# Optimization experiments

Measured on AMD Instinct MI355X. Metric: run time of the kernel, lower is better.

The kernel has to match this reference:

```python
import jax, jax.numpy as jnp
import numpy as np
import math

HEADS = 8
DIM_HEAD = 64

def setup_inputs() -> dict:
    key = jax.random.key(0)
    ks = jax.random.split(key, 6)
    B, L, D = 2, 2048, 512
    Ls = 1936
    inner = HEADS * DIM_HEAD  # 512
    x = jax.random.normal(ks[0], (B, L, D), dtype=jnp.float32)
    positions = jax.random.normal(ks[1], (B, Ls, 2), dtype=jnp.float32) * 10.0
    w_qkv = jax.random.normal(ks[2], (3 * inner, D), dtype=jnp.float32) * (1.0 / math.sqrt(D))
    w_out = jax.random.normal(ks[3], (D, inner), dtype=jnp.float32) * (1.0 / math.sqrt(inner))
    b_out = jnp.zeros((D,), dtype=jnp.float32)
    log_sigma = jnp.full((HEADS,), math.log(3.0), dtype=jnp.float32)
    global_bias = jnp.float32(0.0)
    return {"x": x, "positions": positions, "w_qkv": w_qkv, "w_out": w_out,
            "b_out": b_out, "log_sigma": log_sigma, "global_bias": global_bias,
            "num_spatial": Ls}

def reference(x, positions, w_qkv, w_out, b_out, log_sigma, global_bias, num_spatial):
    B, L, D = x.shape
    H, Dh = HEADS, DIM_HEAD
    scale = Dh ** (-0.5)
    # qkv projection: [B,L,3*H*Dh] -> q,k,v each [B,H,L,Dh]
    qkv = jnp.einsum('bld,ed->ble', x, w_qkv)
    q, k, v = jnp.split(qkv, 3, axis=-1)
    def heads(t):
        return t.reshape(B, L, H, Dh).transpose(0, 2, 1, 3)
    q, k, v = heads(q), heads(k), heads(v)
    attn = jnp.einsum('bhid,bhjd->bhij', q, k) * scale  # [B,H,L,L]
    # Gaussian distance bias on the spatial block, global_bias elsewhere
    Ls = num_spatial
    diff = positions[:, :, None, :] - positions[:, None, :, :]  # [B,Ls,Ls,2]
    dist_sq = jnp.sum(diff * diff, axis=-1)                     # [B,Ls,Ls]
    sigma_sq = jnp.exp(log_sigma) ** 2                          # [H]
    spatial_bias = -dist_sq[:, None] / (2.0 * sigma_sq[None, :, None, None])  # [B,H,Ls,Ls]
    full_bias = jnp.full((B, H, L, L), global_bias, dtype=x.dtype)
    full_bias = full_bias.at[:, :, :Ls, :Ls].set(spatial_bias)
    attn = jax.nn.softmax(attn + full_bias, axis=-1)
    out = jnp.einsum('bhij,bhjd->bhid', attn, v)  # [B,H,L,Dh]
    out = out.transpose(0, 2, 1, 3).reshape(B, L, H * Dh)
    return jnp.einsum('ble,de->bld', out, w_out) + b_out
```

## Files before the change

### kernel.cpp

```cpp
#include <hip/hip_runtime.h>
#include <stdint.h>
#include <stddef.h>

#define NB   2
#define NL   2048
#define ND   512
#define NH   8
#define DH   64
#define LOG2E 1.44269504f
#define NIT  16
#define RG_TOT 32768

typedef __attribute__((ext_vector_type(8))) short bf16x8;
typedef __attribute__((ext_vector_type(4))) float f32x4;

__device__ __forceinline__ unsigned short f2bf(float f) {
  union { float f; unsigned int u; } c; c.f = f;
  unsigned int u = c.u;
  unsigned int r = u + 0x7fffu + ((u >> 16) & 1u);
  return (unsigned short)(r >> 16);
}

__device__ __forceinline__ float fexp2(float x) {
#if __has_builtin(__builtin_amdgcn_exp2f)
  return __builtin_amdgcn_exp2f(x);
#else
  return exp2f(x);
#endif
}

__device__ __forceinline__ void gl_lds16(const unsigned short* g, unsigned short* l) {
#if __has_builtin(__builtin_amdgcn_global_load_lds)
  __builtin_amdgcn_global_load_lds(
      (const __attribute__((address_space(1))) unsigned int*)g,
      (__attribute__((address_space(3))) unsigned int*)l, 16, 0, 0);
#else
  *(uint4*)l = *(const uint4*)g;
#endif
}

#define XC  524288
#define WQC 196608
#define WOC 65536
__global__ void cvt_f32_bf16(const float* __restrict__ x, const float* __restrict__ wq,
                             const float* __restrict__ wo, unsigned short* __restrict__ xb,
                             unsigned short* __restrict__ wqb, unsigned short* __restrict__ wob) {
  int idx = blockIdx.x * 256 + threadIdx.x;
  const float* src; unsigned short* dst; int off;
  if (idx < XC)            { src = x;  dst = xb;  off = idx; }
  else if (idx < XC + WQC) { src = wq; dst = wqb; off = idx - XC; }
  else                     { src = wo; dst = wob; off = idx - XC - WQC; }
  float4 f = ((const float4*)src)[off];
  ushort4 o;
  o.x = f2bf(f.x); o.y = f2bf(f.y); o.z = f2bf(f.z); o.w = f2bf(f.w);
  ((ushort4*)dst)[off] = o;
}

template<int MODE>
__global__ __launch_bounds__(256, 2) void gemm_bf16(
    const unsigned short* __restrict__ A, const unsigned short* __restrict__ Bm,
    const float* __restrict__ bias,
    unsigned short* __restrict__ qo, unsigned short* __restrict__ ko,
    unsigned short* __restrict__ vo, float* __restrict__ out, int K)
{
  __shared__ __align__(16) unsigned short As[128 * 32];
  __shared__ __align__(16) unsigned short Bs[128 * 32];
  const int tid = threadIdx.x, wid = tid >> 6, lane = tid & 63;
  const int quad = lane >> 4, l15 = lane & 15;
  const int m0 = blockIdx.x * 128, n0 = blockIdx.y * 128;
  const int wm = (wid >> 1) * 64, wn = (wid & 1) * 64;

  f32x4 acc[4][4];
#pragma unroll
  for (int a = 0; a < 4; ++a)
#pragma unroll
    for (int b = 0; b < 4; ++b)
#pragma unroll
      for (int z = 0; z < 4; ++z) acc[a][b][z] = 0.f;

  for (int k0 = 0; k0 < K; k0 += 32) {
#pragma unroll
    for (int p = 0; p < 2; ++p) {
      int c = p * 256 + wid * 64 + lane;
      int row = c >> 2, off = c & 3;
      gl_lds16(A  + (size_t)(m0 + row) * K + k0 + off * 8, &As[c * 8]);
      gl_lds16(Bm + (size_t)(n0 + row) * K + k0 + off * 8, &Bs[c * 8]);
    }
    __syncthreads();
    bf16x8 af[4], bfr[4];
#pragma unroll
    for (int mb = 0; mb < 4; ++mb)
      af[mb] = *(const bf16x8*)&As[(wm + mb * 16 + l15) * 32 + quad * 8];
#pragma unroll
    for (int nb = 0; nb < 4; ++nb)
      bfr[nb] = *(const bf16x8*)&Bs[(wn + nb * 16 + l15) * 32 + quad * 8];
#pragma unroll
    for (int mb = 0; mb < 4; ++mb)
#pragma unroll
      for (int nb = 0; nb < 4; ++nb)
        acc[mb][nb] = __builtin_amdgcn_mfma_f32_16x16x32_bf16(af[mb], bfr[nb], acc[mb][nb], 0, 0, 0);
    __syncthreads();
  }

  const float QSCALE = 0.125f * LOG2E;
#pragma unroll
  for (int mb = 0; mb < 4; ++mb) {
#pragma unroll
    for (int r = 0; r < 4; ++r) {
      int m  = m0 + wm + mb * 16 + quad * 4 + r;
      int bb = m >> 11;
      int ll = m & 2047;
#pragma unroll
      for (int nb = 0; nb < 4; ++nb) {
        int n = n0 + wn + nb * 16 + l15;
        float v = acc[mb][nb][r];
        if (MODE == 0) {
          int s  = n >> 9;
          int hh = (n >> 6) & 7;
          int dh = n & 63;
          size_t base = (((size_t)bb * NH + hh) * NL + ll) * DH + dh;
          if (s == 0)      qo[base] = f2bf(v * QSCALE);
          else if (s == 1) ko[base] = f2bf(v);
          else             vo[base] = f2bf(v);
        } else {
          out[(size_t)m * ND + n] = v + bias[n];
        }
      }
    }
  }
}

__global__ __launch_bounds__(256) void transpose_v(const unsigned short* __restrict__ v,
                                                   unsigned short* __restrict__ vT) {
  __shared__ unsigned short T[64][74];
  const int l0 = blockIdx.x * 64;
  const int bh = blockIdx.y;
  const unsigned short* src = v + ((size_t)bh * NL + l0) * DH;
  unsigned short* dst = vT + (size_t)bh * DH * NL;
#pragma unroll
  for (int p = 0; p < 2; ++p) {
    int c = p * 256 + threadIdx.x;
    int row = c >> 3, seg = c & 7;
    *(uint4*)&T[row][seg * 8] = *(const uint4*)(src + row * DH + seg * 8);
  }
  __syncthreads();
#pragma unroll
  for (int p = 0; p < 2; ++p) {
    int c = p * 256 + threadIdx.x;
    int drow = c >> 3, lseg = c & 7;
    unsigned short u[8];
#pragma unroll
    for (int z = 0; z < 8; ++z) u[z] = T[lseg * 8 + z][drow];
    *(uint4*)(dst + (size_t)drow * NL + l0 + lseg * 8) = *(uint4*)u;
  }
}

__global__ __launch_bounds__(256, 2) void flash_kernel(
    const unsigned short* __restrict__ qb, const unsigned short* __restrict__ kb,
    const unsigned short* __restrict__ vTb, const float* __restrict__ positions,
    const float* __restrict__ log_sigma, const float* __restrict__ gbias_p,
    const int* __restrict__ ns_p, float* __restrict__ Pbuf, float* __restrict__ rsbuf)
{
  const int it = blockIdx.x >> 1;
  const int js = blockIdx.x & 1;
  const int h  = blockIdx.y;
  const int b  = blockIdx.z;
  const int i0 = it * 128;
  const int jbase = js * (NL / 2);
  const int Ls = ns_p[0];
  const float gb = gbias_p[0];
  const float sig = __expf(log_sigma[h]);
  const float inv2s2 = 0.5f / (sig * sig);
  const float CI = LOG2E * inv2s2;
  const float A2 = 2.0f * CI;
  const float CG = LOG2E * gb * 0.5f;
  const float C8N = -8.0f * LOG2E;

  const int tid  = threadIdx.x;
  const int wid  = tid >> 6;
  const int lane = tid & 63;
  const int quad = lane >> 4;
  const int l15  = lane & 15;

  __shared__ __align__(16) unsigned short Ks[64][72];
  __shared__ __align__(16) unsigned short Vt[64][72];
  __shared__ __align__(16) unsigned short Ps[128][72];
  __shared__ __align__(16) float4 pjc[64];

  const size_t bh = (size_t)b * NH + h;
  const unsigned short* qbase  = qb  + (bh * NL + i0) * DH;
  const unsigned short* kbase  = kb  + bh * NL * DH;
  const unsigned short* vtbase = vTb + bh * DH * NL;

  bf16x8 af[2][2];
#pragma unroll
  for (int mb = 0; mb < 2; ++mb)
#pragma unroll
    for (int kc = 0; kc < 2; ++kc)
      af[mb][kc] = *(const bf16x8*)(qbase + (size_t)(wid * 32 + mb * 16 + l15) * DH + kc * 32 + quad * 8);

  float pix_[2][4], piy_[2][4], riCm[2][4], ispf[2][4];
#pragma unroll
  for (int mb = 0; mb < 2; ++mb)
#pragma unroll
    for (int r = 0; r < 4; ++r) {
      int ig = i0 + wid * 32 + mb * 16 + quad * 4 + r;
      float px = 0.f, py = 0.f, sf = 0.f, rc = 0.f;
      if (ig < Ls) {
        float2 p2 = *(const float2*)(positions + ((size_t)b * Ls + ig) * 2);
        px = p2.x; py = p2.y; sf = 1.f;
        rc = -(CI * (px * px + py * py)) - CG;
      }
      pix_[mb][r] = px; piy_[mb][r] = py; ispf[mb][r] = sf; riCm[mb][r] = rc;
    }

  f32x4 accO[2][4];
  float rsum[2][4];
#pragma unroll
  for (int mb = 0; mb < 2; ++mb) {
#pragma unroll
    for (int nb = 0; nb < 4; ++nb)
#pragma unroll
      for (int z = 0; z < 4; ++z) accO[mb][nb][z] = 0.f;
#pragma unroll
    for (int r = 0; r < 4; ++r) rsum[mb][r] = 0.f;
  }

  uint4 kr[2], vr[2];
  float2 pr = make_float2(0.f, 0.f);
  {
#pragma unroll
    for (int p = 0; p < 2; ++p) {
      int c = p * 256 + tid;
      int row = c >> 3, off = c & 7;
      kr[p] = *(const uint4*)(kbase  + (size_t)(jbase + row) * DH + off * 8);
      vr[p] = *(const uint4*)(vtbase + (size_t)row * NL + jbase + off * 8);
    }
    if (tid < 64 && (jbase + tid) < Ls)
      pr = *(const float2*)(positions + ((size_t)b * Ls + jbase + tid) * 2);
  }

  for (int jt = 0; jt < 16; ++jt) {
    const int j0 = jbase + jt * 64;
    __syncthreads();

#pragma unroll
    for (int p = 0; p < 2; ++p) {
      int c = p * 256 + tid;
      int row = c >> 3, off = c & 7;
      *(uint4*)&Ks[row][off * 8] = kr[p];
      *(uint4*)&Vt[row][off * 8] = vr[p];
    }
    if (tid < 64) {
      bool jsp = (j0 + tid) < Ls;
      float px = jsp ? pr.x : 0.f, py = jsp ? pr.y : 0.f;
      float rc = jsp ? (-(CI * (px * px + py * py)) - CG) : 0.f;
      pjc[tid] = make_float4(A2 * px, A2 * py, rc, 0.f);
    }
    __syncthreads();

    if (jt + 1 < 16) {
      const int jn = jbase + (jt + 1) * 64;
#pragma unroll
      for (int p = 0; p < 2; ++p) {
        int c = p * 256 + tid;
        int row = c >> 3, off = c & 7;
        kr[p] = *(const uint4*)(kbase  + (size_t)(jn + row) * DH + off * 8);
        vr[p] = *(const uint4*)(vtbase + (size_t)row * NL + jn + off * 8);
      }
      if (tid < 64 && (jn + tid) < Ls)
        pr = *(const float2*)(positions + ((size_t)b * Ls + jn + tid) * 2);
    }

    f32x4 accS[2][4];
#pragma unroll
    for (int mb = 0; mb < 2; ++mb)
#pragma unroll
      for (int nb = 0; nb < 4; ++nb)
#pragma unroll
        for (int z = 0; z < 4; ++z) accS[mb][nb][z] = 0.f;
#pragma unroll
    for (int nb = 0; nb < 4; ++nb) {
      bf16x8 b0 = *(const bf16x8*)&Ks[nb * 16 + l15][quad * 8];
      bf16x8 b1 = *(const bf16x8*)&Ks[nb * 16 + l15][32 + quad * 8];
#pragma unroll
      for (int mb = 0; mb < 2; ++mb) {
        accS[mb][nb] = __builtin_amdgcn_mfma_f32_16x16x32_bf16(af[mb][0], b0, accS[mb][nb], 0, 0, 0);
        accS[mb][nb] = __builtin_amdgcn_mfma_f32_16x16x32_bf16(af[mb][1], b1, accS[mb][nb], 0, 0, 0);
      }
    }

    float4 pc[4]; float jspf_[4];
#pragma unroll
    for (int nb = 0; nb < 4; ++nb) {
      pc[nb] = pjc[nb * 16 + l15];
      jspf_[nb] = ((j0 + nb * 16 + l15) < Ls) ? 1.f : 0.f;
    }
#pragma unroll
    for (int mb = 0; mb < 2; ++mb)
#pragma unroll
      for (int nb = 0; nb < 4; ++nb)
#pragma unroll
        for (int r = 0; r < 4; ++r) {
          float t = accS[mb][nb][r] + C8N;
          t = __builtin_fmaf(ispf[mb][r], pc[nb].z, t);
          t = __builtin_fmaf(jspf_[nb], riCm[mb][r], t);
          t = __builtin_fmaf(piy_[mb][r], pc[nb].y, t);
          t = __builtin_fmaf(pix_[mb][r], pc[nb].x, t);
          float p = fexp2(t);
          rsum[mb][r] += p;
          Ps[wid * 32 + mb * 16 + quad * 4 + r][nb * 16 + l15] = f2bf(p);
        }

    bf16x8 pf[2][2];
#pragma unroll
    for (int mb = 0; mb < 2; ++mb) {
      pf[mb][0] = *(const bf16x8*)&Ps[wid * 32 + mb * 16 + l15][quad * 8];
      pf[mb][1] = *(const bf16x8*)&Ps[wid * 32 + mb * 16 + l15][32 + quad * 8];
    }
#pragma unroll
    for (int nb = 0; nb < 4; ++nb) {
      bf16x8 v0 = *(const bf16x8*)&Vt[nb * 16 + l15][quad * 8];
      bf16x8 v1 = *(const bf16x8*)&Vt[nb * 16 + l15][32 + quad * 8];
#pragma unroll
      for (int mb = 0; mb < 2; ++mb) {
        accO[mb][nb] = __builtin_amdgcn_mfma_f32_16x16x32_bf16(pf[mb][0], v0, accO[mb][nb], 0, 0, 0);
        accO[mb][nb] = __builtin_amdgcn_mfma_f32_16x16x32_bf16(pf[mb][1], v1, accO[mb][nb], 0, 0, 0);
      }
    }
  }

#pragma unroll
  for (int mb = 0; mb < 2; ++mb)
#pragma unroll
    for (int r = 0; r < 4; ++r) {
      float v = rsum[mb][r];
      v += __shfl_xor(v, 1);
      v += __shfl_xor(v, 2);
      v += __shfl_xor(v, 4);
      v += __shfl_xor(v, 8);
      rsum[mb][r] = v;
    }
  const size_t rgbase = (bh * NIT + it) * 128;
  const size_t poff = (size_t)js * RG_TOT * DH;
#pragma unroll
  for (int mb = 0; mb < 2; ++mb)
#pragma unroll
    for (int r = 0; r < 4; ++r) {
      int row = wid * 32 + mb * 16 + quad * 4 + r;
#pragma unroll
      for (int nb = 0; nb < 4; ++nb)
        Pbuf[poff + (rgbase + row) * DH + nb * 16 + l15] = accO[mb][nb][r];
      if (l15 == 0)
        rsbuf[(size_t)js * RG_TOT + rgbase + row] = rsum[mb][r];
    }
}

__global__ __launch_bounds__(256) void combine_kernel(const float* __restrict__ Pbuf,
                                                      const float* __restrict__ rsbuf,
                                                      unsigned short* __restrict__ attnb) {
  int idx = blockIdx.x * 256 + threadIdx.x;
  int rg = idx >> 4, c4 = idx & 15;
  const float4* p4 = (const float4*)Pbuf;
  float4 p0 = p4[(size_t)rg * 16 + c4];
  float4 p1 = p4[(size_t)RG_TOT * 16 + (size_t)rg * 16 + c4];
  float rs = 1.0f / (rsbuf[rg] + rsbuf[RG_TOT + rg]);
  int bhm = rg >> 11;
  int l   = rg & 2047;
  int bb  = bhm >> 3, hh = bhm & 7;
  ushort4 o;
  o.x = f2bf((p0.x + p1.x) * rs);
  o.y = f2bf((p0.y + p1.y) * rs);
  o.z = f2bf((p0.z + p1.z) * rs);
  o.w = f2bf((p0.w + p1.w) * rs);
  *(ushort4*)&attnb[(((size_t)bb * NL + l) * ND) + hh * DH + c4 * 4] = o;
}

extern "C" void kernel_launch(void* const* d_in, const int* in_sizes, int n_in,
                              void* d_out, int out_size, void* d_ws, size_t ws_size,
                              hipStream_t stream) {
  const float* x         = (const float*)d_in[0];
  const float* positions = (const float*)d_in[1];
  const float* w_qkv     = (const float*)d_in[2];
  const float* w_out     = (const float*)d_in[3];
  const float* b_out     = (const float*)d_in[4];
  const float* log_sigma = (const float*)d_in[5];
  const float* gbias     = (const float*)d_in[6];
  const int*   ns        = (const int*)d_in[7];

  unsigned short* ws = (unsigned short*)d_ws;
  unsigned short* xb  = ws;
  unsigned short* wqb = xb  + 2097152;
  unsigned short* wob = wqb + 786432;
  unsigned short* qbf = wob + 262144;
  unsigned short* kbf = qbf + 2097152;
  unsigned short* vbf = kbf + 2097152;
  unsigned short* vTf = vbf + 2097152;
  float* Pbuf  = (float*)(vTf + 2097152);
  float* rsbuf = Pbuf + (size_t)2 * RG_TOT * DH;

  cvt_f32_bf16<<<(XC + WQC + WOC) / 256, 256, 0, stream>>>(x, w_qkv, w_out, xb, wqb, wob);

  dim3 g1(NB * NL / 128, (3 * NH * DH) / 128);
  gemm_bf16<0><<<g1, 256, 0, stream>>>(xb, wqb, nullptr, qbf, kbf, vbf, nullptr, ND);

  dim3 gt(NL / 64, NB * NH);
  transpose_v<<<gt, 256, 0, stream>>>(vbf, vTf);

  dim3 g2(NIT * 2, NH, NB);
  flash_kernel<<<g2, 256, 0, stream>>>(qbf, kbf, vTf, positions, log_sigma, gbias, ns,
                                       Pbuf, rsbuf);

  combine_kernel<<<RG_TOT * 16 / 256, 256, 0, stream>>>(Pbuf, rsbuf, xb);

  dim3 g3(NB * NL / 128, ND / 128);
  gemm_bf16<1><<<g3, 256, 0, stream>>>(xb, wob, b_out, nullptr, nullptr, nullptr,
                                       (float*)d_out, NH * DH);
}
```

Baseline: 167.1 us.

## Transpose flash tiles, drop shared K/V staging, pad positions, vectorize GEMM epilogues

The flash kernel now computes S^T (keys as the MFMA A operand, queries as B) so each lane owns one query row. K and V^T fragments are read straight from global memory instead of being staged through shared memory, which removes both block-wide barriers per tile. Only a small per-wave P buffer stays in LDS. The Gaussian bias is computed directly from a zero-padded positions array that the conversion kernel now builds. Both GEMMs swap operand order so the epilogue writes ushort4/float4 vectors instead of scalars; the trade-off is that global K/V reloads now depend on L2 and lose the register prefetch double-buffering.

```diff
diff --git a/kernel.cpp b/kernel.cpp
--- a/kernel.cpp
+++ b/kernel.cpp
@@ -8,7 +8,6 @@
 #define NH   8
 #define DH   64
 #define LOG2E 1.44269504f
-#define NIT  16
 #define RG_TOT 32768
 
 typedef __attribute__((ext_vector_type(8))) short bf16x8;
@@ -42,18 +41,36 @@
 #define XC  524288
 #define WQC 196608
 #define WOC 65536
+#define TOTC (XC + WQC + WOC)
 __global__ void cvt_f32_bf16(const float* __restrict__ x, const float* __restrict__ wq,
-                             const float* __restrict__ wo, unsigned short* __restrict__ xb,
-                             unsigned short* __restrict__ wqb, unsigned short* __restrict__ wob) {
+                             const float* __restrict__ wo, const float* __restrict__ positions,
+                             const int* __restrict__ ns_p,
+                             unsigned short* __restrict__ xb, unsigned short* __restrict__ wqb,
+                             unsigned short* __restrict__ wob, float* __restrict__ pospad) {
   int idx = blockIdx.x * 256 + threadIdx.x;
-  const float* src; unsigned short* dst; int off;
-  if (idx < XC)            { src = x;  dst = xb;  off = idx; }
-  else if (idx < XC + WQC) { src = wq; dst = wqb; off = idx - XC; }
-  else                     { src = wo; dst = wob; off = idx - XC - WQC; }
-  float4 f = ((const float4*)src)[off];
-  ushort4 o;
-  o.x = f2bf(f.x); o.y = f2bf(f.y); o.z = f2bf(f.z); o.w = f2bf(f.w);
-  ((ushort4*)dst)[off] = o;
+  if (idx < TOTC) {
+    const float* src; unsigned short* dst; int off;
+    if (idx < XC)            { src = x;  dst = xb;  off = idx; }
+    else if (idx < XC + WQC) { src = wq; dst = wqb; off = idx - XC; }
+    else                     { src = wo; dst = wob; off = idx - XC - WQC; }
+    float4 f = ((const float4*)src)[off];
+    ushort4 o;
+    o.x = f2bf(f.x); o.y = f2bf(f.y); o.z = f2bf(f.z); o.w = f2bf(f.w);
+    ((ushort4*)dst)[off] = o;
+  } else {
+    int i2 = idx - TOTC;
+    if (i2 < NB * 1024) {
+      int b = i2 >> 10;
+      int jj = (i2 & 1023) * 2;
+      int Ls = ns_p[0];
+      float4 o = make_float4(0.f, 0.f, 0.f, 0.f);
+      if (jj < Ls) { o.x = positions[((size_t)b * Ls + jj) * 2];
+                     o.y = positions[((size_t)b * Ls + jj) * 2 + 1]; }
+      if (jj + 1 < Ls) { o.z = positions[((size_t)b * Ls + jj + 1) * 2];
+                         o.w = positions[((size_t)b * Ls + jj + 1) * 2 + 1]; }
+      *(float4*)&pospad[((size_t)b * NL + jj) * 2] = o;
+    }
+  }
 }
 
 template<int MODE>
@@ -105,26 +122,35 @@
   const float QSCALE = 0.125f * LOG2E;
 #pragma unroll
   for (int mb = 0; mb < 4; ++mb) {
-#pragma unroll
-    for (int r = 0; r < 4; ++r) {
-      int m  = m0 + wm + mb * 16 + quad * 4 + r;
-      int bb = m >> 11;
-      int ll = m & 2047;
+    int e0 = m0 + wm + mb * 16 + quad * 4;
+    if (MODE == 0) {
+      int s   = e0 >> 9;
+      int hh  = (e0 >> 6) & 7;
+      int dh0 = e0 & 63;
+      unsigned short* dst = (s == 0) ? qo : ((s == 1) ? ko : vo);
+      float sc = (s == 0) ? QSCALE : 1.0f;
 #pragma unroll
       for (int nb = 0; nb < 4; ++nb) {
-        int n = n0 + wn + nb * 16 + l15;
-        float v = acc[mb][nb][r];
-        if (MODE == 0) {
-          int s  = n >> 9;
-          int hh = (n >> 6) & 7;
-          int dh = n & 63;
-          size_t base = (((size_t)bb * NH + hh) * NL + ll) * DH + dh;
-          if (s == 0)      qo[base] = f2bf(v * QSCALE);
-          else if (s == 1) ko[base] = f2bf(v);
-          else             vo[base] = f2bf(v);
-        } else {
-          out[(size_t)m * ND + n] = v + bias[n];
-        }
+        int token = n0 + wn + nb * 16 + l15;
+        int bb = token >> 11, ll = token & 2047;
+        ushort4 o;
+        o.x = f2bf(acc[mb][nb][0] * sc);
+        o.y = f2bf(acc[mb][nb][1] * sc);
+        o.z = f2bf(acc[mb][nb][2] * sc);
+        o.w = f2bf(acc[mb][nb][3] * sc);
+        *(ushort4*)&dst[(((size_t)bb * NH + hh) * NL + ll) * DH + dh0] = o;
+      }
+    } else {
+      float4 bv = *(const float4*)&bias[e0];
+#pragma unroll
+      for (int nb = 0; nb < 4; ++nb) {
+        int token = n0 + wn + nb * 16 + l15;
+        float4 o;
+        o.x = acc[mb][nb][0] + bv.x;
+        o.y = acc[mb][nb][1] + bv.y;
+        o.z = acc[mb][nb][2] + bv.z;
+        o.w = acc[mb][nb][3] + bv.w;
+        *(float4*)&out[(size_t)token * ND + e0] = o;
       }
     }
   }
@@ -157,7 +183,7 @@
 
 __global__ __launch_bounds__(256, 2) void flash_kernel(
     const unsigned short* __restrict__ qb, const unsigned short* __restrict__ kb,
-    const unsigned short* __restrict__ vTb, const float* __restrict__ positions,
+    const unsigned short* __restrict__ vTb, const float* __restrict__ pospad,
     const float* __restrict__ log_sigma, const float* __restrict__ gbias_p,
     const int* __restrict__ ns_p, float* __restrict__ Pbuf, float* __restrict__ rsbuf)
 {
@@ -168,12 +194,10 @@
   const int i0 = it * 128;
   const int jbase = js * (NL / 2);
   const int Ls = ns_p[0];
-  const float gb = gbias_p[0];
+  const float gb  = gbias_p[0];
   const float sig = __expf(log_sigma[h]);
-  const float inv2s2 = 0.5f / (sig * sig);
-  const float CI = LOG2E * inv2s2;
-  const float A2 = 2.0f * CI;
-  const float CG = LOG2E * gb * 0.5f;
+  const float CI  = LOG2E * 0.5f / (sig * sig);
+  const float LGB = LOG2E * gb;
   const float C8N = -8.0f * LOG2E;
 
   const int tid  = threadIdx.x;
@@ -182,178 +206,122 @@
   const int quad = lane >> 4;
   const int l15  = lane & 15;
 
-  __shared__ __align__(16) unsigned short Ks[64][72];
-  __shared__ __align__(16) unsigned short Vt[64][72];
-  __shared__ __align__(16) unsigned short Ps[128][72];
-  __shared__ __align__(16) float4 pjc[64];
+  __shared__ __align__(16) unsigned short Pls[4][2][16][72];
 
   const size_t bh = (size_t)b * NH + h;
-  const unsigned short* qbase  = qb  + (bh * NL + i0) * DH;
+  const unsigned short* qbase  = qb  + (bh * NL + i0 + wid * 32) * DH;
   const unsigned short* kbase  = kb  + bh * NL * DH;
   const unsigned short* vtbase = vTb + bh * DH * NL;
-
-  bf16x8 af[2][2];
-#pragma unroll
-  for (int mb = 0; mb < 2; ++mb)
+  const float* posb = pospad + (size_t)b * NL * 2;
+
+  bf16x8 qf[2][2];
+  float pix[2], piy[2], ispf[2];
+#pragma unroll
+  for (int ib = 0; ib < 2; ++ib) {
 #pragma unroll
     for (int kc = 0; kc < 2; ++kc)
-      af[mb][kc] = *(const bf16x8*)(qbase + (size_t)(wid * 32 + mb * 16 + l15) * DH + kc * 32 + quad * 8);
-
-  float pix_[2][4], piy_[2][4], riCm[2][4], ispf[2][4];
-#pragma unroll
-  for (int mb = 0; mb < 2; ++mb)
-#pragma unroll
-    for (int r = 0; r < 4; ++r) {
-      int ig = i0 + wid * 32 + mb * 16 + quad * 4 + r;
-      float px = 0.f, py = 0.f, sf = 0.f, rc = 0.f;
-      if (ig < Ls) {
-        float2 p2 = *(const float2*)(positions + ((size_t)b * Ls + ig) * 2);
-        px = p2.x; py = p2.y; sf = 1.f;
-        rc = -(CI * (px * px + py * py)) - CG;
-      }
-      pix_[mb][r] = px; piy_[mb][r] = py; ispf[mb][r] = sf; riCm[mb][r] = rc;
-    }
-
-  f32x4 accO[2][4];
-  float rsum[2][4];
-#pragma unroll
-  for (int mb = 0; mb < 2; ++mb) {
-#pragma unroll
-    for (int nb = 0; nb < 4; ++nb)
-#pragma unroll
-      for (int z = 0; z < 4; ++z) accO[mb][nb][z] = 0.f;
-#pragma unroll
-    for (int r = 0; r < 4; ++r) rsum[mb][r] = 0.f;
-  }
-
-  uint4 kr[2], vr[2];
-  float2 pr = make_float2(0.f, 0.f);
-  {
-#pragma unroll
-    for (int p = 0; p < 2; ++p) {
-      int c = p * 256 + tid;
-      int row = c >> 3, off = c & 7;
-      kr[p] = *(const uint4*)(kbase  + (size_t)(jbase + row) * DH + off * 8);
-      vr[p] = *(const uint4*)(vtbase + (size_t)row * NL + jbase + off * 8);
-    }
-    if (tid < 64 && (jbase + tid) < Ls)
-      pr = *(const float2*)(positions + ((size_t)b * Ls + jbase + tid) * 2);
-  }
+      qf[ib][kc] = *(const bf16x8*)(qbase + (size_t)(ib * 16 + l15) * DH + kc * 32 + quad * 8);
+    int ig = i0 + wid * 32 + ib * 16 + l15;
+    float2 p2 = *(const float2*)(posb + (size_t)ig * 2);
+    pix[ib] = p2.x; piy[ib] = p2.y;
+    ispf[ib] = (ig < Ls) ? 1.f : 0.f;
+  }
+
+  f32x4 accO[4][2];
+  float rsum[2];
+#pragma unroll
+  for (int d = 0; d < 4; ++d)
+#pragma unroll
+    for (int ib = 0; ib < 2; ++ib)
+#pragma unroll
+      for (int z = 0; z < 4; ++z) accO[d][ib][z] = 0.f;
+  rsum[0] = 0.f; rsum[1] = 0.f;
 
   for (int jt = 0; jt < 16; ++jt) {
     const int j0 = jbase + jt * 64;
-    __syncthreads();
-
-#pragma unroll
-    for (int p = 0; p < 2; ++p) {
-      int c = p * 256 + tid;
-      int row = c >> 3, off = c & 7;
-      *(uint4*)&Ks[row][off * 8] = kr[p];
-      *(uint4*)&Vt[row][off * 8] = vr[p];
-    }
-    if (tid < 64) {
-      bool jsp = (j0 + tid) < Ls;
-      float px = jsp ? pr.x : 0.f, py = jsp ? pr.y : 0.f;
-      float rc = jsp ? (-(CI * (px * px + py * py)) - CG) : 0.f;
-      pjc[tid] = make_float4(A2 * px, A2 * py, rc, 0.f);
-    }
-    __syncthreads();
-
-    if (jt + 1 < 16) {
-      const int jn = jbase + (jt + 1) * 64;
-#pragma unroll
-      for (int p = 0; p < 2; ++p) {
-        int c = p * 256 + tid;
-        int row = c >> 3, off = c & 7;
-        kr[p] = *(const uint4*)(kbase  + (size_t)(jn + row) * DH + off * 8);
-        vr[p] = *(const uint4*)(vtbase + (size_t)row * NL + jn + off * 8);
-      }
-      if (tid < 64 && (jn + tid) < Ls)
-        pr = *(const float2*)(positions + ((size_t)b * Ls + jn + tid) * 2);
-    }
-
-    f32x4 accS[2][4];
-#pragma unroll
-    for (int mb = 0; mb < 2; ++mb)
-#pragma unroll
-      for (int nb = 0; nb < 4; ++nb)
-#pragma unroll
-        for (int z = 0; z < 4; ++z) accS[mb][nb][z] = 0.f;
-#pragma unroll
-    for (int nb = 0; nb < 4; ++nb) {
-      bf16x8 b0 = *(const bf16x8*)&Ks[nb * 16 + l15][quad * 8];
-      bf16x8 b1 = *(const bf16x8*)&Ks[nb * 16 + l15][32 + quad * 8];
-#pragma unroll
-      for (int mb = 0; mb < 2; ++mb) {
-        accS[mb][nb] = __builtin_amdgcn_mfma_f32_16x16x32_bf16(af[mb][0], b0, accS[mb][nb], 0, 0, 0);
-        accS[mb][nb] = __builtin_amdgcn_mfma_f32_16x16x32_bf16(af[mb][1], b1, accS[mb][nb], 0, 0, 0);
-      }
-    }
-
-    float4 pc[4]; float jspf_[4];
-#pragma unroll
-    for (int nb = 0; nb < 4; ++nb) {
-      pc[nb] = pjc[nb * 16 + l15];
-      jspf_[nb] = ((j0 + nb * 16 + l15) < Ls) ? 1.f : 0.f;
-    }
-#pragma unroll
-    for (int mb = 0; mb < 2; ++mb)
-#pragma unroll
-      for (int nb = 0; nb < 4; ++nb)
+
+    bf16x8 kf[4][2];
+#pragma unroll
+    for (int jb = 0; jb < 4; ++jb)
+#pragma unroll
+      for (int kc = 0; kc < 2; ++kc)
+        kf[jb][kc] = *(const bf16x8*)(kbase + (size_t)(j0 + jb * 16 + l15) * DH + kc * 32 + quad * 8);
+
+    f32x4 accS[4][2];
+#pragma unroll
+    for (int jb = 0; jb < 4; ++jb)
+#pragma unroll
+      for (int ib = 0; ib < 2; ++ib) {
+#pragma unroll
+        for (int z = 0; z < 4; ++z) accS[jb][ib][z] = 0.f;
+        accS[jb][ib] = __builtin_amdgcn_mfma_f32_16x16x32_bf16(kf[jb][0], qf[ib][0], accS[jb][ib], 0, 0, 0);
+        accS[jb][ib] = __builtin_amdgcn_mfma_f32_16x16x32_bf16(kf[jb][1], qf[ib][1], accS[jb][ib], 0, 0, 0);
+      }
+
+#pragma unroll
+    for (int jb = 0; jb < 4; ++jb) {
+      int jrow = j0 + jb * 16 + quad * 4;
+      float4 pA = *(const float4*)(posb + (size_t)jrow * 2);
+      float4 pB = *(const float4*)(posb + (size_t)jrow * 2 + 4);
+      float px[4] = {pA.x, pA.z, pB.x, pB.z};
+      float py[4] = {pA.y, pA.w, pB.y, pB.w};
+      float jok[4];
+#pragma unroll
+      for (int r = 0; r < 4; ++r) jok[r] = (jrow + r < Ls) ? 1.f : 0.f;
+#pragma unroll
+      for (int ib = 0; ib < 2; ++ib) {
+        float p[4];
 #pragma unroll
         for (int r = 0; r < 4; ++r) {
-          float t = accS[mb][nb][r] + C8N;
-          t = __builtin_fmaf(ispf[mb][r], pc[nb].z, t);
-          t = __builtin_fmaf(jspf_[nb], riCm[mb][r], t);
-          t = __builtin_fmaf(piy_[mb][r], pc[nb].y, t);
-          t = __builtin_fmaf(pix_[mb][r], pc[nb].x, t);
-          float p = fexp2(t);
-          rsum[mb][r] += p;
-          Ps[wid * 32 + mb * 16 + quad * 4 + r][nb * 16 + l15] = f2bf(p);
+          float dx = pix[ib] - px[r];
+          float dy = piy[ib] - py[r];
+          float d2 = __builtin_fmaf(dx, dx, dy * dy);
+          float u  = __builtin_fmaf(CI, d2, LGB);
+          float m  = jok[r] * ispf[ib];
+          float t  = __builtin_fmaf(-m, u, accS[jb][ib][r] + C8N);
+          p[r] = fexp2(t);
         }
-
-    bf16x8 pf[2][2];
-#pragma unroll
-    for (int mb = 0; mb < 2; ++mb) {
-      pf[mb][0] = *(const bf16x8*)&Ps[wid * 32 + mb * 16 + l15][quad * 8];
-      pf[mb][1] = *(const bf16x8*)&Ps[wid * 32 + mb * 16 + l15][32 + quad * 8];
-    }
-#pragma unroll
-    for (int nb = 0; nb < 4; ++nb) {
-      bf16x8 v0 = *(const bf16x8*)&Vt[nb * 16 + l15][quad * 8];
-      bf16x8 v1 = *(const bf16x8*)&Vt[nb * 16 + l15][32 + quad * 8];
-#pragma unroll
-      for (int mb = 0; mb < 2; ++mb) {
-        accO[mb][nb] = __builtin_amdgcn_mfma_f32_16x16x32_bf16(pf[mb][0], v0, accO[mb][nb], 0, 0, 0);
-        accO[mb][nb] = __builtin_amdgcn_mfma_f32_16x16x32_bf16(pf[mb][1], v1, accO[mb][nb], 0, 0, 0);
-      }
-    }
-  }
-
-#pragma unroll
-  for (int mb = 0; mb < 2; ++mb)
-#pragma unroll
-    for (int r = 0; r < 4; ++r) {
-      float v = rsum[mb][r];
-      v += __shfl_xor(v, 1);
-      v += __shfl_xor(v, 2);
-      v += __shfl_xor(v, 4);
-      v += __shfl_xor(v, 8);
-      rsum[mb][r] = v;
-    }
-  const size_t rgbase = (bh * NIT + it) * 128;
-  const size_t poff = (size_t)js * RG_TOT * DH;
-#pragma unroll
-  for (int mb = 0; mb < 2; ++mb)
-#pragma unroll
-    for (int r = 0; r < 4; ++r) {
-      int row = wid * 32 + mb * 16 + quad * 4 + r;
-#pragma unroll
-      for (int nb = 0; nb < 4; ++nb)
-        Pbuf[poff + (rgbase + row) * DH + nb * 16 + l15] = accO[mb][nb][r];
-      if (l15 == 0)
-        rsbuf[(size_t)js * RG_TOT + rgbase + row] = rsum[mb][r];
-    }
+        rsum[ib] += (p[0] + p[1]) + (p[2] + p[3]);
+        uint2 w;
+        w.x = (uint32_t)f2bf(p[0]) | ((uint32_t)f2bf(p[1]) << 16);
+        w.y = (uint32_t)f2bf(p[2]) | ((uint32_t)f2bf(p[3]) << 16);
+        *(uint2*)&Pls[wid][ib][l15][jb * 16 + quad * 4] = w;
+      }
+    }
+
+    bf16x8 pbf[2][2];
+#pragma unroll
+    for (int ib = 0; ib < 2; ++ib)
+#pragma unroll
+      for (int pp = 0; pp < 2; ++pp)
+        pbf[ib][pp] = *(const bf16x8*)&Pls[wid][ib][l15][pp * 32 + quad * 8];
+#pragma unroll
+    for (int dhb = 0; dhb < 4; ++dhb)
+#pragma unroll
+      for (int pp = 0; pp < 2; ++pp) {
+        bf16x8 vf = *(const bf16x8*)(vtbase + (size_t)(dhb * 16 + l15) * NL + j0 + pp * 32 + quad * 8);
+#pragma unroll
+        for (int ib = 0; ib < 2; ++ib)
+          accO[dhb][ib] = __builtin_amdgcn_mfma_f32_16x16x32_bf16(vf, pbf[ib][pp], accO[dhb][ib], 0, 0, 0);
+      }
+  }
+
+#pragma unroll
+  for (int ib = 0; ib < 2; ++ib) {
+    float v = rsum[ib];
+    v += __shfl_xor(v, 16);
+    v += __shfl_xor(v, 32);
+    int ig = i0 + wid * 32 + ib * 16 + l15;
+    if (quad == 0)
+      rsbuf[(size_t)js * RG_TOT + bh * NL + ig] = v;
+#pragma unroll
+    for (int dhb = 0; dhb < 4; ++dhb) {
+      float4 o;
+      o.x = accO[dhb][ib][0]; o.y = accO[dhb][ib][1];
+      o.z = accO[dhb][ib][2]; o.w = accO[dhb][ib][3];
+      *(float4*)&Pbuf[((size_t)js * RG_TOT + bh * NL + ig) * DH + dhb * 16 + quad * 4] = o;
+    }
+  }
 }
 
 __global__ __launch_bounds__(256) void combine_kernel(const float* __restrict__ Pbuf,
@@ -396,24 +364,26 @@
   unsigned short* kbf = qbf + 2097152;
   unsigned short* vbf = kbf + 2097152;
   unsigned short* vTf = vbf + 2097152;
-  float* Pbuf  = (float*)(vTf + 2097152);
-  float* rsbuf = Pbuf + (size_t)2 * RG_TOT * DH;
-
-  cvt_f32_bf16<<<(XC + WQC + WOC) / 256, 256, 0, stream>>>(x, w_qkv, w_out, xb, wqb, wob);
-
-  dim3 g1(NB * NL / 128, (3 * NH * DH) / 128);
-  gemm_bf16<0><<<g1, 256, 0, stream>>>(xb, wqb, nullptr, qbf, kbf, vbf, nullptr, ND);
+  float* Pbuf   = (float*)(vTf + 2097152);
+  float* rsbuf  = Pbuf + (size_t)2 * RG_TOT * DH;
+  float* pospad = rsbuf + 2 * RG_TOT;
+
+  cvt_f32_bf16<<<(TOTC + NB * 1024 + 255) / 256, 256, 0, stream>>>(
+      x, w_qkv, w_out, positions, ns, xb, wqb, wob, pospad);
+
+  dim3 g1((3 * NH * DH) / 128, NB * NL / 128);
+  gemm_bf16<0><<<g1, 256, 0, stream>>>(wqb, xb, nullptr, qbf, kbf, vbf, nullptr, ND);
 
   dim3 gt(NL / 64, NB * NH);
   transpose_v<<<gt, 256, 0, stream>>>(vbf, vTf);
 
-  dim3 g2(NIT * 2, NH, NB);
-  flash_kernel<<<g2, 256, 0, stream>>>(qbf, kbf, vTf, positions, log_sigma, gbias, ns,
+  dim3 g2((NL / 128) * 2, NH, NB);
+  flash_kernel<<<g2, 256, 0, stream>>>(qbf, kbf, vTf, pospad, log_sigma, gbias, ns,
                                        Pbuf, rsbuf);
 
   combine_kernel<<<RG_TOT * 16 / 256, 256, 0, stream>>>(Pbuf, rsbuf, xb);
 
-  dim3 g3(NB * NL / 128, ND / 128);
-  gemm_bf16<1><<<g3, 256, 0, stream>>>(xb, wob, b_out, nullptr, nullptr, nullptr,
+  dim3 g3(ND / 128, NB * NL / 128);
+  gemm_bf16<1><<<g3, 256, 0, stream>>>(wob, xb, b_out, nullptr, nullptr, nullptr,
                                        (float*)d_out, NH * DH);
 }
```

Measured after the change: 199.4 us. +19.3%, slower.
